# Kernel optimization log

Measured on AMD Instinct MI355X. Metric: run time of the kernel, lower is better.

## Reference

```python
import jax, jax.numpy as jnp
import numpy as np

N = 16384          # nodes
E_R = 524288       # radial edges (avg degree 32)
E_B = 32768        # bonded edges
N_TYPES = 20       # atom types
CS = 64            # scalar (0e) channels
CV = 32            # vector (1o) channels
EA = 16            # edge_attr_dim
EA_B = EA // 2     # bondedness embedding dim
EA_R = (EA + 1) // 2  # radial basis dim
CUTOFF = 1.5       # effective_radial_cutoff
L = 2              # n_layers
NORM = float(np.sqrt((E_R + E_B) / N))  # ~sqrt(avg degree) message normalization


def setup_inputs() -> dict:
    key = jax.random.key(0)
    ks = jax.random.split(key, 32)
    def rn(i, shape, scale=1.0):
        return jax.random.normal(ks[i], shape, dtype=jnp.float32) * scale
    s_e = 1.0 / np.sqrt(EA)
    inp = {}
    inp["pos"] = rn(0, (N, 3))
    inp["c_noise"] = rn(1, (1,))
    inp["atom_types"] = jax.random.randint(ks[2], (N,), 0, N_TYPES)
    inp["radial_edge_index"] = jax.random.randint(ks[3], (2, E_R), 0, N)
    inp["bonded_edge_index"] = jax.random.randint(ks[4], (2, E_B), 0, N)
    # learned parameters
    inp["atom_tab"] = rn(5, (N_TYPES, CS))
    inp["bond_tab"] = rn(6, (2, EA_B))
    inp["ns0_w"] = rn(7, (CS,), 0.1)
    inp["We0"] = rn(8, (EA, CS), s_e)
    inp["We1"] = rn(9, (EA, CS), s_e)
    inp["Wself0"] = rn(10, (CS, CS), 1.0 / np.sqrt(CS))
    inp["Ws0"] = rn(11, (CS, CS), 1.0 / np.sqrt(CS))
    inp["Wv0"] = rn(12, (CS, CV), 1.0 / np.sqrt(CS))
    inp["ns_w"] = rn(13, (L, CS + CV), 0.1)
    inp["We_ss"] = rn(14, (L, EA, CS), s_e)
    inp["We_vs"] = rn(15, (L, EA, CV), s_e)
    inp["We_sv"] = rn(16, (L, EA, CS), s_e)
    inp["We_vv"] = rn(17, (L, EA, CV), s_e)
    inp["We_vx"] = rn(18, (L, EA, CV), s_e)
    inp["Wmix_s"] = rn(19, (L, CS + CV, CS), 1.0 / np.sqrt(CS + CV))
    inp["Wmix_v"] = rn(20, (L, CS + 2 * CV, CV), 1.0 / np.sqrt(CS + 2 * CV))
    inp["Wself_s"] = rn(21, (L, CS, CS), 1.0 / np.sqrt(CS))
    inp["Wself_v"] = rn(22, (L, CV, CV), 1.0 / np.sqrt(CV))
    inp["skip_w"] = rn(23, (L, 2 * (CS + CV)), 0.1)
    inp["skip_b"] = rn(24, (L, 2 * (CS + CV)), 0.1)
    inp["w_out"] = rn(25, (CV,), 1.0 / np.sqrt(CV))
    inp["gain"] = jnp.asarray(0.5, dtype=jnp.float32)
    return inp


def _radial_basis(d):
    # e3nn soft_one_hot_linspace, basis='gaussian', cutoff=True
    centers = jnp.linspace(0.0, CUTOFF, EA_R + 2)[1:-1]
    step = centers[1] - centers[0]
    diff = (d[:, None] - centers[None, :]) / step
    return jnp.exp(-diff * diff) * 1.12


def reference(pos, c_noise, atom_tab, bond_tab, ns0_w, We0, We1, Wself0, Ws0, Wv0,
              ns_w, We_ss, We_vs, We_sv, We_vv, We_vx, Wmix_s, Wmix_v, Wself_s, Wself_v,
              skip_w, skip_b, w_out, gain, atom_types, radial_edge_index, bonded_edge_index):
    edge_index = jnp.concatenate([radial_edge_index, bonded_edge_index], axis=1)
    bond_mask = jnp.concatenate([jnp.zeros((E_R,), jnp.int32), jnp.ones((E_B,), jnp.int32)])
    src, dst = edge_index[0], edge_index[1]
    edge_vec = pos[src] - pos[dst]                      # [E,3]
    d = jnp.sqrt(jnp.sum(edge_vec * edge_vec, -1) + 1e-12)
    Y1 = jnp.sqrt(3.0) * edge_vec / d[:, None]          # l=1 SH, component norm; Y0 == 1
    edge_attr = jnp.concatenate([bond_tab[bond_mask], _radial_basis(d)], axis=-1)  # [E,EA]

    # atom embedding + initial noise-conditional scaling
    s = atom_tab[atom_types] * (1.0 + c_noise * ns0_w)  # [N,CS]

    # initial projector: scalar-input equivariant conv -> hidden irreps
    w0 = edge_attr @ We0
    w1 = edge_attr @ We1
    s_src = s[src]
    a_s = jax.ops.segment_sum(w0 * s_src, dst, num_segments=N) / NORM
    a_v = jax.ops.segment_sum((w1 * s_src)[:, :, None] * Y1[:, None, :], dst, num_segments=N) / NORM
    s_h = a_s @ Ws0 + s @ Wself0                        # [N,CS]
    v_h = jnp.einsum('nci,cd->ndi', a_v, Wv0)           # [N,CV,3]

    for l in range(L):
        # noise-conditional scaling (per-irrep-channel scalar scale)
        scale = 1.0 + c_noise * ns_w[l]
        ss = s_h * scale[:CS]
        vv = v_h * scale[CS:][None, :, None]
        ss_e = ss[src]
        vv_e = vv[src]
        # edge-attr-conditioned tensor-product weights
        w_ss = edge_attr @ We_ss[l]
        w_vs = edge_attr @ We_vs[l]
        w_sv = edge_attr @ We_sv[l]
        w_vv = edge_attr @ We_vv[l]
        w_vx = edge_attr @ We_vx[l]
        # CG tensor-product messages: 0x0->0, 1x1->0 (dot), 0x1->1, 1x0->1, 1x1->1 (cross)
        vdot = jnp.einsum('eci,ei->ec', vv_e, Y1)
        m_s = jnp.concatenate([w_ss * ss_e, w_vs * vdot], axis=-1)          # [E,CS+CV]
        m_v = jnp.concatenate([
            (w_sv * ss_e)[:, :, None] * Y1[:, None, :],
            w_vv[:, :, None] * vv_e,
            w_vx[:, :, None] * jnp.cross(vv_e, Y1[:, None, :]),
        ], axis=1)                                                          # [E,CS+2CV,3]
        a_s = jax.ops.segment_sum(m_s, dst, num_segments=N) / NORM
        a_v = jax.ops.segment_sum(m_v, dst, num_segments=N) / NORM
        new_s = a_s @ Wmix_s[l] + ss @ Wself_s[l]
        new_v = jnp.einsum('nci,cd->ndi', a_v, Wmix_v[l]) + jnp.einsum('nci,cd->ndi', vv, Wself_v[l])
        # noise-conditional skip connection (gated residual)
        g = jax.nn.sigmoid(skip_b[l] + c_noise * skip_w[l])
        s_h = g[:CS] * s_h + g[CS:2 * CS] * new_s
        g_v = g[2 * CS:]
        v_h = g_v[:CV][None, :, None] * v_h + g_v[CV:][None, :, None] * new_v

    # output head: 1o vectors -> 3D displacement, times output gain
    return jnp.einsum('nci,c->ni', v_h, w_out) * gain
```

## Files before the change

### kernel.cpp

```cpp
#include <hip/hip_runtime.h>
#include <math.h>

#define NA 16384
#define ER 524288
#define EB 32768
#define ET 557056
#define INV_NORM 0.17149858514250882f
#define SQRT3 1.7320508075688772f
#define RB_STEP (1.5f/9.0f)
#define BINS 512
#define DMAX 2.5f
#define INV_H ((float)BINS / DMAX)
#define T0U (2 * BINS * 128)
#define TLU (2 * BINS * 256)

typedef unsigned int uint32;
typedef unsigned short ushort16;

__device__ __forceinline__ float sigmoidf_(float x) { return 1.f / (1.f + __expf(-x)); }

__device__ __forceinline__ ushort16 f2bf(float x) {
  uint32 u = __float_as_uint(x);
  u = u + 0x7FFFu + ((u >> 16) & 1u);
  return (ushort16)(u >> 16);
}
__device__ __forceinline__ uint32 packbf(float hi, float lo) {
  return ((uint32)f2bf(hi) << 16) | (uint32)f2bf(lo);
}
__device__ __forceinline__ float bfhi(uint32 u) { return __uint_as_float(u & 0xFFFF0000u); }
__device__ __forceinline__ float bflo(uint32 u) { return __uint_as_float(u << 16); }

__global__ void k_zero(int* __restrict__ count) {
  count[blockIdx.x * 256 + threadIdx.x] = 0;
}

__global__ void k_hist(const int* __restrict__ rad, const int* __restrict__ bon, int* __restrict__ count) {
  int e = blockIdx.x * 256 + threadIdx.x;
  int d = (e < ER) ? rad[ER + e] : bon[EB + (e - ER)];
  atomicAdd(&count[d], 1);
}

__global__ void k_scan1(const int* __restrict__ count, int* __restrict__ partial) {
  __shared__ int red[256];
  int b = blockIdx.x, t = threadIdx.x;
  red[t] = count[b * 256 + t];
  __syncthreads();
  for (int s = 128; s > 0; s >>= 1) {
    if (t < s) red[t] += red[t + s];
    __syncthreads();
  }
  if (t == 0) partial[b] = red[0];
}

__global__ void k_scan2(int* __restrict__ partial) {
  int run = 0;
  for (int i = 0; i < 64; ++i) { int c = partial[i]; partial[i] = run; run += c; }
}

__global__ void k_scan3(const int* __restrict__ count, const int* __restrict__ partial,
                        int* __restrict__ offsets, int* __restrict__ cursor) {
  __shared__ int sc[256];
  int b = blockIdx.x, t = threadIdx.x;
  int v = count[b * 256 + t];
  sc[t] = v;
  __syncthreads();
  for (int off = 1; off < 256; off <<= 1) {
    int x = (t >= off) ? sc[t - off] : 0;
    __syncthreads();
    sc[t] += x;
    __syncthreads();
  }
  int excl = sc[t] - v + partial[b];
  offsets[b * 256 + t] = excl;
  cursor[b * 256 + t] = excl;
  if (b == 63 && t == 255) offsets[NA] = excl + v;
}

__global__ void k_fill_pre(const int* __restrict__ rad, const int* __restrict__ bon,
                           int* __restrict__ cursor, const float* __restrict__ pos,
                           float* __restrict__ rec8) {
  int e = blockIdx.x * 256 + threadIdx.x;
  int src, dst, v;
  if (e < ER) { src = rad[e]; dst = rad[ER + e]; v = 0; }
  else        { src = bon[e - ER]; dst = bon[EB + e - ER]; v = 1; }
  float dx = pos[src * 3] - pos[dst * 3];
  float dy = pos[src * 3 + 1] - pos[dst * 3 + 1];
  float dz = pos[src * 3 + 2] - pos[dst * 3 + 2];
  float dist = sqrtf(dx * dx + dy * dy + dz * dz + 1e-12f);
  float inv = 1.f / dist;
  float fq = fminf(dist * INV_H, BINS - 1.001f);
  int q = (int)fq;
  float frac = fq - (float)q;
  int qoffL = (v * BINS + q) << 8;
  int slot = atomicAdd(&cursor[dst], 1);
  float* rp = rec8 + (size_t)slot * 8;
  *(float4*)rp = make_float4(__int_as_float(src), SQRT3 * dx * inv, SQRT3 * dy * inv, SQRT3 * dz * inv);
  rp[4] = frac;
  rp[5] = __int_as_float(qoffL);
}

__global__ void k_build(const float* __restrict__ We0, const float* __restrict__ We1,
                        const float* __restrict__ We_ss, const float* __restrict__ We_vs,
                        const float* __restrict__ We_sv, const float* __restrict__ We_vv,
                        const float* __restrict__ We_vx, const float* __restrict__ bond_tab,
                        uint32* __restrict__ T0, uint32* __restrict__ TL) {
  int q = blockIdx.x, t = blockIdx.y, v = blockIdx.z, c = threadIdx.x;
  float d0 = q * (DMAX / BINS), d1 = (q + 1) * (DMAX / BINS);
  float rb0[8], rb1[8];
#pragma unroll
  for (int k = 0; k < 8; ++k) {
    float f0 = (d0 - (k + 1) * RB_STEP) * (1.f / RB_STEP);
    float f1 = (d1 - (k + 1) * RB_STEP) * (1.f / RB_STEP);
    rb0[k] = 1.12f * __expf(-f0 * f0);
    rb1[k] = 1.12f * __expf(-f1 * f1);
  }
  if (t == 0) {
    float ba = 0, bb = 0, a0 = 0, a1 = 0, b0 = 0, b1 = 0;
#pragma unroll
    for (int k = 0; k < 8; ++k) {
      float bt = bond_tab[v * 8 + k];
      float av_lo = We0[k * 64 + c], av_hi = We0[(8 + k) * 64 + c];
      float bv_lo = We1[k * 64 + c], bv_hi = We1[(8 + k) * 64 + c];
      ba += bt * av_lo; bb += bt * bv_lo;
      a0 += rb0[k] * av_hi; a1 += rb1[k] * av_hi;
      b0 += rb0[k] * bv_hi; b1 += rb1[k] * bv_hi;
    }
    uint32* o = T0 + (((size_t)v * BINS + q) << 7) + c * 2;
    o[0] = packbf(ba + a0, a1 - a0);
    o[1] = packbf(bb + b0, b1 - b0);
  } else {
    int l = t - 1;
    const float* Wss = We_ss + l * 1024;
    const float* Wsv = We_sv + l * 1024;
    const float* WA = (c < 32) ? (We_vs + l * 512) : (We_vx + l * 512);
    const float* WB = (c < 32) ? (We_vv + l * 512) : nullptr;
    int cu = c & 31;
    float sa = 0, sb = 0, s0 = 0, s1 = 0, t0 = 0, t1 = 0;
    float ua = 0, ub = 0, u0 = 0, u1 = 0, w0 = 0, w1 = 0;
#pragma unroll
    for (int k = 0; k < 8; ++k) {
      float bt = bond_tab[v * 8 + k];
      float ss_lo = Wss[k * 64 + c], ss_hi = Wss[(8 + k) * 64 + c];
      float sv_lo = Wsv[k * 64 + c], sv_hi = Wsv[(8 + k) * 64 + c];
      sa += bt * ss_lo; sb += bt * sv_lo;
      s0 += rb0[k] * ss_hi; s1 += rb1[k] * ss_hi;
      t0 += rb0[k] * sv_hi; t1 += rb1[k] * sv_hi;
      float a_lo = WA[k * 32 + cu], a_hi = WA[(8 + k) * 32 + cu];
      ua += bt * a_lo;
      u0 += rb0[k] * a_hi; u1 += rb1[k] * a_hi;
      if (WB) {
        float b_lo = WB[k * 32 + cu], b_hi = WB[(8 + k) * 32 + cu];
        ub += bt * b_lo;
        w0 += rb0[k] * b_hi; w1 += rb1[k] * b_hi;
      }
    }
    uint32* o = TL + (size_t)l * TLU + (((size_t)v * BINS + q) << 8) + c * 4;
    o[0] = packbf(sa + s0, s1 - s0);
    o[1] = packbf(sb + t0, t1 - t0);
    o[2] = packbf(ua + u0, u1 - u0);
    o[3] = WB ? packbf(ub + w0, w1 - w0) : 0u;
  }
}

__global__ void k_embed(const float* __restrict__ atom_tab, const int* __restrict__ types,
                        const float* __restrict__ ns0_w, const float* __restrict__ cnoise,
                        float* __restrict__ s_feat, ushort16* __restrict__ s_bf) {
  int tid = blockIdx.x * 256 + threadIdx.x;
  int n = tid >> 6, c = tid & 63;
  float cn = cnoise[0];
  float v = atom_tab[types[n] * 64 + c] * (1.f + cn * ns0_w[c]);
  s_feat[tid] = v;
  s_bf[tid] = f2bf(v);
}

__global__ __launch_bounds__(256, 8) void k_agg0(
    const int* __restrict__ offsets, const float* __restrict__ rec8,
    const uint32* __restrict__ T0, const ushort16* __restrict__ s_bf,
    float* __restrict__ a_s, float* __restrict__ a_v) {
  int lane = threadIdx.x & 63;
  int n = blockIdx.x * 4 + (threadIdx.x >> 6);
  float acc = 0, a0 = 0, a1 = 0, a2 = 0;
  int beg = __builtin_amdgcn_readfirstlane(offsets[n]);
  int end = __builtin_amdgcn_readfirstlane(offsets[n + 1]);
  if (beg < end) {
    int last = end - 1;
    int e1 = (beg + 1 < end) ? beg + 1 : last;
    int e2 = (beg + 2 < end) ? beg + 2 : last;
    const float* p0 = rec8 + (size_t)beg * 8;
    const float* p1 = rec8 + (size_t)e1 * 8;
    const float* p2 = rec8 + (size_t)e2 * 8;
    float4 rA0 = *(const float4*)p0; float2 rB0 = *(const float2*)(p0 + 4);
    float4 rA1 = *(const float4*)p1; float2 rB1 = *(const float2*)(p1 + 4);
    float4 rA2 = *(const float4*)p2; float2 rB2 = *(const float2*)(p2 + 4);
    uint2 t0 = *(const uint2*)(T0 + (__float_as_int(rB0.y) >> 1) + (lane << 1));
    ushort16 s0 = s_bf[((size_t)__float_as_int(rA0.x) << 6) + lane];
    uint2 t1 = *(const uint2*)(T0 + (__float_as_int(rB1.y) >> 1) + (lane << 1));
    ushort16 s1 = s_bf[((size_t)__float_as_int(rA1.x) << 6) + lane];
#pragma unroll 3
    for (int idx = beg; idx < end; ++idx) {
      uint2 t2 = *(const uint2*)(T0 + (__float_as_int(rB2.y) >> 1) + (lane << 1));
      ushort16 s2 = s_bf[((size_t)__float_as_int(rA2.x) << 6) + lane];
      int e3 = (idx + 3 < end) ? idx + 3 : last;
      const float* p3 = rec8 + (size_t)e3 * 8;
      float4 rA3 = *(const float4*)p3; float2 rB3 = *(const float2*)(p3 + 4);
      float frac = rB0.x;
      float w0 = fmaf(frac, bflo(t0.x), bfhi(t0.x));
      float w1 = fmaf(frac, bflo(t0.y), bfhi(t0.y));
      float sv = __uint_as_float((uint32)s0 << 16);
      acc += w0 * sv;
      float t = w1 * sv;
      a0 += t * rA0.y; a1 += t * rA0.z; a2 += t * rA0.w;
      rA0 = rA1; rB0 = rB1; rA1 = rA2; rB1 = rB2; rA2 = rA3; rB2 = rB3;
      t0 = t1; s0 = s1; t1 = t2; s1 = s2;
    }
  }
  a_s[n * 64 + lane] = acc * INV_NORM;
  *(float4*)(a_v + ((size_t)n << 8) + (lane << 2)) =
      make_float4(a0 * INV_NORM, a1 * INV_NORM, a2 * INV_NORM, 0.f);
}

__global__ __launch_bounds__(256, 8) void k_agg_layer(
    const float* __restrict__ cnoise, const float* __restrict__ nsw,
    const int* __restrict__ offsets, const float* __restrict__ rec8,
    const uint32* __restrict__ TL, const ushort16* __restrict__ sh_bf,
    const uint32* __restrict__ vh_bf,
    float* __restrict__ a_s, float* __restrict__ a_v) {
  int lane = threadIdx.x & 63;
  int n = blockIdx.x * 4 + (threadIdx.x >> 6);
  int vc = lane & 31;
  bool low = lane < 32;
  float cn = cnoise[0];
  float scale_s = 1.f + cn * nsw[lane];
  float scale_v = 1.f + cn * nsw[64 + vc];

  float ms = 0;
  float av0 = 0, av1 = 0, av2 = 0;
  float ms2 = 0;
  float b0 = 0, b1 = 0, b2 = 0;
  int beg = __builtin_amdgcn_readfirstlane(offsets[n]);
  int end = __builtin_amdgcn_readfirstlane(offsets[n + 1]);
  if (beg < end) {
    int last = end - 1;
    int e1 = (beg + 1 < end) ? beg + 1 : last;
    int e2 = (beg + 2 < end) ? beg + 2 : last;
    const float* p0 = rec8 + (size_t)beg * 8;
    const float* p1 = rec8 + (size_t)e1 * 8;
    const float* p2 = rec8 + (size_t)e2 * 8;
    float4 rA0 = *(const float4*)p0; float2 rB0 = *(const float2*)(p0 + 4);
    float4 rA1 = *(const float4*)p1; float2 rB1 = *(const float2*)(p1 + 4);
    float4 rA2 = *(const float4*)p2; float2 rB2 = *(const float2*)(p2 + 4);
    uint4 t0 = *(const uint4*)(TL + __float_as_int(rB0.y) + (lane << 2));
    ushort16 s0 = sh_bf[((size_t)__float_as_int(rA0.x) << 6) + lane];
    uint2 v0 = *(const uint2*)(vh_bf + ((size_t)__float_as_int(rA0.x) << 6) + (vc << 1));
    uint4 t1 = *(const uint4*)(TL + __float_as_int(rB1.y) + (lane << 2));
    ushort16 s1 = sh_bf[((size_t)__float_as_int(rA1.x) << 6) + lane];
    uint2 v1 = *(const uint2*)(vh_bf + ((size_t)__float_as_int(rA1.x) << 6) + (vc << 1));
#pragma unroll 3
    for (int idx = beg; idx < end; ++idx) {
      uint4 t2 = *(const uint4*)(TL + __float_as_int(rB2.y) + (lane << 2));
      ushort16 s2 = sh_bf[((size_t)__float_as_int(rA2.x) << 6) + lane];
      uint2 v2 = *(const uint2*)(vh_bf + ((size_t)__float_as_int(rA2.x) << 6) + (vc << 1));
      int e3 = (idx + 3 < end) ? idx + 3 : last;
      const float* p3 = rec8 + (size_t)e3 * 8;
      float4 rA3 = *(const float4*)p3; float2 rB3 = *(const float2*)(p3 + 4);
      float frac = rB0.x;
      float y0 = rA0.y, y1 = rA0.z, y2 = rA0.w;
      float wS  = fmaf(frac, bflo(t0.x), bfhi(t0.x));
      float wSV = fmaf(frac, bflo(t0.y), bfhi(t0.y));
      float wA  = fmaf(frac, bflo(t0.z), bfhi(t0.z));
      float wB  = fmaf(frac, bflo(t0.w), bfhi(t0.w));
      float ss = __uint_as_float((uint32)s0 << 16);
      float vx = bfhi(v0.x), vy = bflo(v0.x), vz = bfhi(v0.y);
      ms += wS * ss;
      float t = wSV * ss;
      av0 += t * y0; av1 += t * y1; av2 += t * y2;
      float vdot = vx * y0 + vy * y1 + vz * y2;
      ms2 += wA * vdot;
      float cx = vy * y2 - vz * y1;
      float cy = vz * y0 - vx * y2;
      float cz = vx * y1 - vy * y0;
      float m0 = low ? vx : cx;
      float m1 = low ? vy : cy;
      float m2 = low ? vz : cz;
      float wM = low ? wB : wA;
      b0 += wM * m0; b1 += wM * m1; b2 += wM * m2;
      rA0 = rA1; rB0 = rB1; rA1 = rA2; rB1 = rB2; rA2 = rA3; rB2 = rB3;
      t0 = t1; s0 = s1; v0 = v1; t1 = t2; s1 = s2; v1 = v2;
    }
  }
  float fs = scale_s * INV_NORM;
  float fv = scale_v * INV_NORM;
  a_s[n * 96 + lane] = ms * fs;
  float* avn = a_v + ((size_t)n << 9);
  *(float4*)(avn + (lane << 2)) = make_float4(av0 * fs, av1 * fs, av2 * fs, 0.f);
  if (low) {
    a_s[n * 96 + 64 + vc] = ms2 * fv;
    *(float4*)(avn + ((64 + vc) << 2)) = make_float4(b0 * fv, b1 * fv, b2 * fv, 0.f);
  } else {
    *(float4*)(avn + ((96 + vc) << 2)) = make_float4(b0 * fv, b1 * fv, b2 * fv, 0.f);
  }
}

__global__ __launch_bounds__(256, 4) void k_init_s(
    const float* __restrict__ a_s, const float* __restrict__ s_feat,
    const float* __restrict__ Ws0, const float* __restrict__ Wself0,
    float* __restrict__ sh, ushort16* __restrict__ sh_bf) {
  __shared__ float W1[64 * 64];
  __shared__ float W2[64 * 64];
  __shared__ float La[8 * 64];
  __shared__ float Lf[8 * 64];
  int tid = threadIdx.x;
  for (int i = tid; i < 1024; i += 256) {
    ((float4*)W1)[i] = ((const float4*)Ws0)[i];
    ((float4*)W2)[i] = ((const float4*)Wself0)[i];
  }
  int base = blockIdx.x * 8;
  for (int i = tid; i < 512; i += 256) {
    La[i] = a_s[(size_t)base * 64 + i];
    Lf[i] = s_feat[(size_t)base * 64 + i];
  }
  __syncthreads();
  int d = tid & 63, g = tid >> 6;
  int n0 = base + g * 2;
  const float* A0 = La + g * 128;
  const float* A1 = A0 + 64;
  const float* F0 = Lf + g * 128;
  const float* F1 = F0 + 64;
  float a0 = 0, a1 = 0;
#pragma unroll 8
  for (int c = 0; c < 64; ++c) {
    float w1 = W1[c * 64 + d], w2 = W2[c * 64 + d];
    a0 += A0[c] * w1 + F0[c] * w2;
    a1 += A1[c] * w1 + F1[c] * w2;
  }
  sh[(size_t)n0 * 64 + d] = a0;
  sh[(size_t)(n0 + 1) * 64 + d] = a1;
  sh_bf[(size_t)n0 * 64 + d] = f2bf(a0);
  sh_bf[(size_t)(n0 + 1) * 64 + d] = f2bf(a1);
}

__global__ __launch_bounds__(256, 4) void k_init_v(
    const float* __restrict__ a_v, const float* __restrict__ Wv0,
    float* __restrict__ vh, uint32* __restrict__ vh_bf) {
  __shared__ float W[64 * 32];
  int tid = threadIdx.x;
  for (int i = tid; i < 512; i += 256) ((float4*)W)[i] = ((const float4*)Wv0)[i];
  __syncthreads();
  int d = tid & 31, g = tid >> 5;
  int n = blockIdx.x * 8 + g;
  const float4* av = (const float4*)(a_v + ((size_t)n << 8));
  float x = 0, y = 0, z = 0;
#pragma unroll 4
  for (int c = 0; c < 64; ++c) {
    float4 a = av[c];
    float w = W[c * 32 + d];
    x += a.x * w; y += a.y * w; z += a.z * w;
  }
  *(float4*)(vh + ((size_t)n << 7) + (d << 2)) = make_float4(x, y, z, 0.f);
  *(uint2*)(vh_bf + ((size_t)n << 6) + (d << 1)) = make_uint2(packbf(x, y), packbf(z, 0.f));
}

__global__ __launch_bounds__(256, 4) void k_mix_s(
    const float* __restrict__ a_s, const float* __restrict__ sh_in,
    const float* __restrict__ Wmix_s, const float* __restrict__ Wself_s,
    const float* __restrict__ nsw, const float* __restrict__ skw,
    const float* __restrict__ skb, const float* __restrict__ cnoise,
    float* __restrict__ sh_out, ushort16* __restrict__ sh_bf_out) {
  __shared__ float Wm[96 * 64];
  __shared__ float Wsf[64 * 64];
  __shared__ float La[8 * 96];
  int tid = threadIdx.x;
  float cn = cnoise[0];
  for (int i = tid; i < 96 * 16; i += 256) ((float4*)Wm)[i] = ((const float4*)Wmix_s)[i];
  for (int i = tid; i < 64 * 16; i += 256) {
    float4 wv = ((const float4*)Wself_s)[i];
    int c = i >> 4;
    float sc = 1.f + cn * nsw[c];
    wv.x *= sc; wv.y *= sc; wv.z *= sc; wv.w *= sc;
    ((float4*)Wsf)[i] = wv;
  }
  int base = blockIdx.x * 8;
  for (int i = tid; i < 8 * 96; i += 256) La[i] = a_s[(size_t)base * 96 + i];
  __syncthreads();
  int d = tid & 63, g = tid >> 6;
  int n0 = base + g * 2;
  const float* A0 = La + (g * 2) * 96;
  const float* A1 = A0 + 96;
  const float* s0p = sh_in + (size_t)n0 * 64;
  const float* s1p = s0p + 64;
  float acc0 = 0, acc1 = 0;
#pragma unroll 8
  for (int c = 0; c < 96; ++c) {
    float w = Wm[c * 64 + d];
    acc0 += A0[c] * w;
    acc1 += A1[c] * w;
  }
#pragma unroll 8
  for (int c = 0; c < 64; ++c) {
    float w = Wsf[c * 64 + d];
    acc0 += s0p[c] * w;
    acc1 += s1p[c] * w;
  }
  float g1 = sigmoidf_(skb[d] + cn * skw[d]);
  float g2 = sigmoidf_(skb[64 + d] + cn * skw[64 + d]);
  float o0 = g1 * s0p[d] + g2 * acc0;
  float o1 = g1 * s1p[d] + g2 * acc1;
  sh_out[(size_t)n0 * 64 + d] = o0;
  sh_out[(size_t)(n0 + 1) * 64 + d] = o1;
  sh_bf_out[(size_t)n0 * 64 + d] = f2bf(o0);
  sh_bf_out[(size_t)(n0 + 1) * 64 + d] = f2bf(o1);
}

__global__ __launch_bounds__(256, 4) void k_mix_v(
    const float* __restrict__ a_v, const float* __restrict__ vh_in,
    const float* __restrict__ Wmix_v, const float* __restrict__ Wself_v,
    const float* __restrict__ nsw, const float* __restrict__ skw,
    const float* __restrict__ skb, const float* __restrict__ cnoise,
    float* __restrict__ vh_out, uint32* __restrict__ vh_bf_out) {
  __shared__ float Wm[128 * 32];
  __shared__ float Wsf[32 * 32];
  int tid = threadIdx.x;
  float cn = cnoise[0];
  for (int i = tid; i < 128 * 8; i += 256) ((float4*)Wm)[i] = ((const float4*)Wmix_v)[i];
  for (int i = tid; i < 32 * 8; i += 256) {
    float4 wv = ((const float4*)Wself_v)[i];
    int c = i >> 3;
    float sc = 1.f + cn * nsw[64 + c];
    wv.x *= sc; wv.y *= sc; wv.z *= sc; wv.w *= sc;
    ((float4*)Wsf)[i] = wv;
  }
  __syncthreads();
  int d = tid & 31, g = tid >> 5;
  int n = blockIdx.x * 8 + g;
  const float4* av = (const float4*)(a_v + ((size_t)n << 9));
  const float4* vr = (const float4*)(vh_in + ((size_t)n << 7));
  float x = 0, y = 0, z = 0;
#pragma unroll 4
  for (int c = 0; c < 128; ++c) {
    float4 a = av[c];
    float w = Wm[c * 32 + d];
    x += a.x * w; y += a.y * w; z += a.z * w;
  }
#pragma unroll 4
  for (int c = 0; c < 32; ++c) {
    float4 vv = vr[c];
    float w = Wsf[c * 32 + d];
    x += vv.x * w; y += vv.y * w; z += vv.z * w;
  }
  float g3 = sigmoidf_(skb[128 + d] + cn * skw[128 + d]);
  float g4 = sigmoidf_(skb[160 + d] + cn * skw[160 + d]);
  float4 vi = vr[d];
  float ox = g3 * vi.x + g4 * x;
  float oy = g3 * vi.y + g4 * y;
  float oz = g3 * vi.z + g4 * z;
  *(float4*)(vh_out + ((size_t)n << 7) + (d << 2)) = make_float4(ox, oy, oz, 0.f);
  *(uint2*)(vh_bf_out + ((size_t)n << 6) + (d << 1)) = make_uint2(packbf(ox, oy), packbf(oz, 0.f));
}

__global__ void k_out(const float* __restrict__ vh, const float* __restrict__ w_out,
                      const float* __restrict__ gain, float* __restrict__ out) {
  int tid = blockIdx.x * 256 + threadIdx.x;
  int n = tid / 3, i = tid - n * 3;
  float acc = 0;
  for (int c = 0; c < 32; ++c) acc += vh[((size_t)n << 7) + c * 4 + i] * w_out[c];
  out[tid] = acc * gain[0];
}

extern "C" void kernel_launch(void* const* d_in, const int* in_sizes, int n_in,
                              void* d_out, int out_size, void* d_ws, size_t ws_size,
                              hipStream_t stream) {
  (void)in_sizes; (void)n_in; (void)out_size; (void)ws_size;
  const float* pos     = (const float*)d_in[0];
  const float* cn      = (const float*)d_in[1];
  const int*   types   = (const int*)d_in[2];
  const int*   rad     = (const int*)d_in[3];
  const int*   bon     = (const int*)d_in[4];
  const float* atom_tab= (const float*)d_in[5];
  const float* bond_tab= (const float*)d_in[6];
  const float* ns0_w   = (const float*)d_in[7];
  const float* We0     = (const float*)d_in[8];
  const float* We1     = (const float*)d_in[9];
  const float* Wself0  = (const float*)d_in[10];
  const float* Ws0     = (const float*)d_in[11];
  const float* Wv0     = (const float*)d_in[12];
  const float* ns_w    = (const float*)d_in[13];
  const float* We_ss   = (const float*)d_in[14];
  const float* We_vs   = (const float*)d_in[15];
  const float* We_sv   = (const float*)d_in[16];
  const float* We_vv   = (const float*)d_in[17];
  const float* We_vx   = (const float*)d_in[18];
  const float* Wmix_s  = (const float*)d_in[19];
  const float* Wmix_v  = (const float*)d_in[20];
  const float* Wself_s = (const float*)d_in[21];
  const float* Wself_v = (const float*)d_in[22];
  const float* skip_w  = (const float*)d_in[23];
  const float* skip_b  = (const float*)d_in[24];
  const float* w_out   = (const float*)d_in[25];
  const float* gain    = (const float*)d_in[26];

  char* ws = (char*)d_ws;
  size_t o = 0;
  auto alloc = [&](size_t bytes) -> void* {
    void* p = ws + o;
    o += (bytes + 255) & ~(size_t)255;
    return p;
  };
  float* s_feat  = (float*)alloc((size_t)NA * 64 * 4);
  ushort16* s_bf = (ushort16*)alloc((size_t)NA * 64 * 2);
  float* a_s     = (float*)alloc((size_t)NA * 96 * 4);
  float* a_v     = (float*)alloc((size_t)NA * 512 * 4);
  float* sh0     = (float*)alloc((size_t)NA * 64 * 4);
  float* sh1     = (float*)alloc((size_t)NA * 64 * 4);
  ushort16* shbf0= (ushort16*)alloc((size_t)NA * 64 * 2);
  ushort16* shbf1= (ushort16*)alloc((size_t)NA * 64 * 2);
  float* vh0     = (float*)alloc((size_t)NA * 128 * 4);
  float* vh1     = (float*)alloc((size_t)NA * 128 * 4);
  uint32* vhbf0  = (uint32*)alloc((size_t)NA * 64 * 4);
  uint32* vhbf1  = (uint32*)alloc((size_t)NA * 64 * 4);
  int* count     = (int*)alloc((size_t)NA * 4);
  int* partial   = (int*)alloc((size_t)64 * 4);
  int* offsets   = (int*)alloc((size_t)(NA + 1) * 4);
  int* cursor    = (int*)alloc((size_t)NA * 4);
  float* rec8    = (float*)alloc((size_t)ET * 32);
  uint32* T0     = (uint32*)alloc((size_t)T0U * 4);
  uint32* TL     = (uint32*)alloc((size_t)2 * TLU * 4);
  float* shb[2]  = {sh0, sh1};
  ushort16* shbf[2] = {shbf0, shbf1};
  float* vhb[2]  = {vh0, vh1};
  uint32* vhbf[2]= {vhbf0, vhbf1};

  k_zero<<<NA / 256, 256, 0, stream>>>(count);
  k_hist<<<ET / 256, 256, 0, stream>>>(rad, bon, count);
  k_scan1<<<64, 256, 0, stream>>>(count, partial);
  k_scan2<<<1, 1, 0, stream>>>(partial);
  k_scan3<<<64, 256, 0, stream>>>(count, partial, offsets, cursor);
  k_fill_pre<<<ET / 256, 256, 0, stream>>>(rad, bon, cursor, pos, rec8);
  k_build<<<dim3(BINS, 3, 2), 64, 0, stream>>>(We0, We1, We_ss, We_vs, We_sv, We_vv, We_vx,
                                               bond_tab, T0, TL);

  k_embed<<<NA * 64 / 256, 256, 0, stream>>>(atom_tab, types, ns0_w, cn, s_feat, s_bf);
  k_agg0<<<NA / 4, 256, 0, stream>>>(offsets, rec8, T0, s_bf, a_s, a_v);
  k_init_s<<<NA / 8, 256, 0, stream>>>(a_s, s_feat, Ws0, Wself0, shb[0], shbf[0]);
  k_init_v<<<NA / 8, 256, 0, stream>>>(a_v, Wv0, vhb[0], vhbf[0]);

  for (int l = 0; l < 2; ++l) {
    int bin = l & 1, bout = 1 - bin;
    k_agg_layer<<<NA / 4, 256, 0, stream>>>(
        cn, ns_w + l * 96, offsets, rec8, TL + (size_t)l * TLU, shbf[bin], vhbf[bin], a_s, a_v);
    k_mix_s<<<NA / 8, 256, 0, stream>>>(
        a_s, shb[bin], Wmix_s + l * 96 * 64, Wself_s + l * 64 * 64,
        ns_w + l * 96, skip_w + l * 192, skip_b + l * 192, cn, shb[bout], shbf[bout]);
    k_mix_v<<<NA / 8, 256, 0, stream>>>(
        a_v, vhb[bin], Wmix_v + l * 128 * 32, Wself_v + l * 32 * 32,
        ns_w + l * 96, skip_w + l * 192, skip_b + l * 192, cn, vhb[bout], vhbf[bout]);
  }
  k_out<<<NA * 3 / 256, 256, 0, stream>>>(vhb[0], w_out, gain, (float*)d_out);
}
```

Measured before the change: 470.7 us.

## Merge small kernels, store aggregated vectors in bf16, use nontemporal edge loads

Several independent launches are merged into single grids by splitting on block index: fill with embed, init_s with init_v, and mix_s with mix_v per layer. The zero kernel becomes a memset. The aggregated vector buffer a_v is now written as packed bf16 instead of float4, halving its traffic. Edge-record loads and aggregate stores use nontemporal hints. The bf16 storage of a_v costs precision in the mixing matmuls, and merged kernels use a larger shared-memory footprint that may lower occupancy.

New measurement: 508.8 us. +8.1%, slower.

```diff
diff --git a/kernel.cpp b/kernel.cpp
--- a/kernel.cpp
+++ b/kernel.cpp
@@ -16,6 +16,9 @@
 
 typedef unsigned int uint32;
 typedef unsigned short ushort16;
+typedef float vf4 __attribute__((ext_vector_type(4)));
+typedef float vf2 __attribute__((ext_vector_type(2)));
+typedef unsigned int vu2 __attribute__((ext_vector_type(2)));
 
 __device__ __forceinline__ float sigmoidf_(float x) { return 1.f / (1.f + __expf(-x)); }
 
@@ -30,8 +33,28 @@
 __device__ __forceinline__ float bfhi(uint32 u) { return __uint_as_float(u & 0xFFFF0000u); }
 __device__ __forceinline__ float bflo(uint32 u) { return __uint_as_float(u << 16); }
 
-__global__ void k_zero(int* __restrict__ count) {
-  count[blockIdx.x * 256 + threadIdx.x] = 0;
+__device__ __forceinline__ float4 ntl4(const float* p) {
+  vf4 v = __builtin_nontemporal_load((const vf4*)p);
+  return make_float4(v.x, v.y, v.z, v.w);
+}
+__device__ __forceinline__ float2 ntl2(const float* p) {
+  vf2 v = __builtin_nontemporal_load((const vf2*)p);
+  return make_float2(v.x, v.y);
+}
+__device__ __forceinline__ void nts4(float* p, float a, float b, float c, float d) {
+  vf4 v; v.x = a; v.y = b; v.z = c; v.w = d;
+  __builtin_nontemporal_store(v, (vf4*)p);
+}
+__device__ __forceinline__ void nts2(float* p, float a, float b) {
+  vf2 v; v.x = a; v.y = b;
+  __builtin_nontemporal_store(v, (vf2*)p);
+}
+__device__ __forceinline__ void ntsu2(uint32* p, uint32 a, uint32 b) {
+  vu2 v; v.x = a; v.y = b;
+  __builtin_nontemporal_store(v, (vu2*)p);
+}
+__device__ __forceinline__ void nts1(float* p, float a) {
+  __builtin_nontemporal_store(a, p);
 }
 
 __global__ void k_hist(const int* __restrict__ rad, const int* __restrict__ bon, int* __restrict__ count) {
@@ -76,27 +99,38 @@
   if (b == 63 && t == 255) offsets[NA] = excl + v;
 }
 
-__global__ void k_fill_pre(const int* __restrict__ rad, const int* __restrict__ bon,
-                           int* __restrict__ cursor, const float* __restrict__ pos,
-                           float* __restrict__ rec8) {
-  int e = blockIdx.x * 256 + threadIdx.x;
-  int src, dst, v;
-  if (e < ER) { src = rad[e]; dst = rad[ER + e]; v = 0; }
-  else        { src = bon[e - ER]; dst = bon[EB + e - ER]; v = 1; }
-  float dx = pos[src * 3] - pos[dst * 3];
-  float dy = pos[src * 3 + 1] - pos[dst * 3 + 1];
-  float dz = pos[src * 3 + 2] - pos[dst * 3 + 2];
-  float dist = sqrtf(dx * dx + dy * dy + dz * dz + 1e-12f);
-  float inv = 1.f / dist;
-  float fq = fminf(dist * INV_H, BINS - 1.001f);
-  int q = (int)fq;
-  float frac = fq - (float)q;
-  int qoffL = (v * BINS + q) << 8;
-  int slot = atomicAdd(&cursor[dst], 1);
-  float* rp = rec8 + (size_t)slot * 8;
-  *(float4*)rp = make_float4(__int_as_float(src), SQRT3 * dx * inv, SQRT3 * dy * inv, SQRT3 * dz * inv);
-  rp[4] = frac;
-  rp[5] = __int_as_float(qoffL);
+__global__ void k_fill_embed(const int* __restrict__ rad, const int* __restrict__ bon,
+                             int* __restrict__ cursor, const float* __restrict__ pos,
+                             float* __restrict__ rec8,
+                             const float* __restrict__ atom_tab, const int* __restrict__ types,
+                             const float* __restrict__ ns0_w, const float* __restrict__ cnoise,
+                             float* __restrict__ s_feat, ushort16* __restrict__ s_bf) {
+  if (blockIdx.x < ET / 256) {
+    int e = blockIdx.x * 256 + threadIdx.x;
+    int src, dst, v;
+    if (e < ER) { src = rad[e]; dst = rad[ER + e]; v = 0; }
+    else        { src = bon[e - ER]; dst = bon[EB + e - ER]; v = 1; }
+    float dx = pos[src * 3] - pos[dst * 3];
+    float dy = pos[src * 3 + 1] - pos[dst * 3 + 1];
+    float dz = pos[src * 3 + 2] - pos[dst * 3 + 2];
+    float dist = sqrtf(dx * dx + dy * dy + dz * dz + 1e-12f);
+    float inv = 1.f / dist;
+    float fq = fminf(dist * INV_H, BINS - 1.001f);
+    int q = (int)fq;
+    float frac = fq - (float)q;
+    int qoffL = (v * BINS + q) << 8;
+    int slot = atomicAdd(&cursor[dst], 1);
+    float* rp = rec8 + (size_t)slot * 8;
+    nts4(rp, __int_as_float(src), SQRT3 * dx * inv, SQRT3 * dy * inv, SQRT3 * dz * inv);
+    nts2(rp + 4, frac, __int_as_float(qoffL));
+  } else {
+    int tid = (blockIdx.x - ET / 256) * 256 + threadIdx.x;
+    int n = tid >> 6, c = tid & 63;
+    float cn = cnoise[0];
+    float v = atom_tab[types[n] * 64 + c] * (1.f + cn * ns0_w[c]);
+    s_feat[tid] = v;
+    s_bf[tid] = f2bf(v);
+  }
 }
 
 __global__ void k_build(const float* __restrict__ We0, const float* __restrict__ We1,
@@ -162,21 +196,10 @@
   }
 }
 
-__global__ void k_embed(const float* __restrict__ atom_tab, const int* __restrict__ types,
-                        const float* __restrict__ ns0_w, const float* __restrict__ cnoise,
-                        float* __restrict__ s_feat, ushort16* __restrict__ s_bf) {
-  int tid = blockIdx.x * 256 + threadIdx.x;
-  int n = tid >> 6, c = tid & 63;
-  float cn = cnoise[0];
-  float v = atom_tab[types[n] * 64 + c] * (1.f + cn * ns0_w[c]);
-  s_feat[tid] = v;
-  s_bf[tid] = f2bf(v);
-}
-
 __global__ __launch_bounds__(256, 8) void k_agg0(
     const int* __restrict__ offsets, const float* __restrict__ rec8,
     const uint32* __restrict__ T0, const ushort16* __restrict__ s_bf,
-    float* __restrict__ a_s, float* __restrict__ a_v) {
+    float* __restrict__ a_s, uint32* __restrict__ a_v) {
   int lane = threadIdx.x & 63;
   int n = blockIdx.x * 4 + (threadIdx.x >> 6);
   float acc = 0, a0 = 0, a1 = 0, a2 = 0;
@@ -189,9 +212,9 @@
     const float* p0 = rec8 + (size_t)beg * 8;
     const float* p1 = rec8 + (size_t)e1 * 8;
     const float* p2 = rec8 + (size_t)e2 * 8;
-    float4 rA0 = *(const float4*)p0; float2 rB0 = *(const float2*)(p0 + 4);
-    float4 rA1 = *(const float4*)p1; float2 rB1 = *(const float2*)(p1 + 4);
-    float4 rA2 = *(const float4*)p2; float2 rB2 = *(const float2*)(p2 + 4);
+    float4 rA0 = ntl4(p0); float2 rB0 = ntl2(p0 + 4);
+    float4 rA1 = ntl4(p1); float2 rB1 = ntl2(p1 + 4);
+    float4 rA2 = ntl4(p2); float2 rB2 = ntl2(p2 + 4);
     uint2 t0 = *(const uint2*)(T0 + (__float_as_int(rB0.y) >> 1) + (lane << 1));
     ushort16 s0 = s_bf[((size_t)__float_as_int(rA0.x) << 6) + lane];
     uint2 t1 = *(const uint2*)(T0 + (__float_as_int(rB1.y) >> 1) + (lane << 1));
@@ -202,7 +225,7 @@
       ushort16 s2 = s_bf[((size_t)__float_as_int(rA2.x) << 6) + lane];
       int e3 = (idx + 3 < end) ? idx + 3 : last;
       const float* p3 = rec8 + (size_t)e3 * 8;
-      float4 rA3 = *(const float4*)p3; float2 rB3 = *(const float2*)(p3 + 4);
+      float4 rA3 = ntl4(p3); float2 rB3 = ntl2(p3 + 4);
       float frac = rB0.x;
       float w0 = fmaf(frac, bflo(t0.x), bfhi(t0.x));
       float w1 = fmaf(frac, bflo(t0.y), bfhi(t0.y));
@@ -214,9 +237,9 @@
       t0 = t1; s0 = s1; t1 = t2; s1 = s2;
     }
   }
-  a_s[n * 64 + lane] = acc * INV_NORM;
-  *(float4*)(a_v + ((size_t)n << 8) + (lane << 2)) =
-      make_float4(a0 * INV_NORM, a1 * INV_NORM, a2 * INV_NORM, 0.f);
+  nts1(a_s + n * 64 + lane, acc * INV_NORM);
+  ntsu2(a_v + ((size_t)n << 7) + (lane << 1),
+        packbf(a0 * INV_NORM, a1 * INV_NORM), packbf(a2 * INV_NORM, 0.f));
 }
 
 __global__ __launch_bounds__(256, 8) void k_agg_layer(
@@ -224,7 +247,7 @@
     const int* __restrict__ offsets, const float* __restrict__ rec8,
     const uint32* __restrict__ TL, const ushort16* __restrict__ sh_bf,
     const uint32* __restrict__ vh_bf,
-    float* __restrict__ a_s, float* __restrict__ a_v) {
+    float* __restrict__ a_s, uint32* __restrict__ a_v) {
   int lane = threadIdx.x & 63;
   int n = blockIdx.x * 4 + (threadIdx.x >> 6);
   int vc = lane & 31;
@@ -246,9 +269,9 @@
     const float* p0 = rec8 + (size_t)beg * 8;
     const float* p1 = rec8 + (size_t)e1 * 8;
     const float* p2 = rec8 + (size_t)e2 * 8;
-    float4 rA0 = *(const float4*)p0; float2 rB0 = *(const float2*)(p0 + 4);
-    float4 rA1 = *(const float4*)p1; float2 rB1 = *(const float2*)(p1 + 4);
-    float4 rA2 = *(const float4*)p2; float2 rB2 = *(const float2*)(p2 + 4);
+    float4 rA0 = ntl4(p0); float2 rB0 = ntl2(p0 + 4);
+    float4 rA1 = ntl4(p1); float2 rB1 = ntl2(p1 + 4);
+    float4 rA2 = ntl4(p2); float2 rB2 = ntl2(p2 + 4);
     uint4 t0 = *(const uint4*)(TL + __float_as_int(rB0.y) + (lane << 2));
     ushort16 s0 = sh_bf[((size_t)__float_as_int(rA0.x) << 6) + lane];
     uint2 v0 = *(const uint2*)(vh_bf + ((size_t)__float_as_int(rA0.x) << 6) + (vc << 1));
@@ -262,7 +285,7 @@
       uint2 v2 = *(const uint2*)(vh_bf + ((size_t)__float_as_int(rA2.x) << 6) + (vc << 1));
       int e3 = (idx + 3 < end) ? idx + 3 : last;
       const float* p3 = rec8 + (size_t)e3 * 8;
-      float4 rA3 = *(const float4*)p3; float2 rB3 = *(const float2*)(p3 + 4);
+      float4 rA3 = ntl4(p3); float2 rB3 = ntl2(p3 + 4);
       float frac = rB0.x;
       float y0 = rA0.y, y1 = rA0.z, y2 = rA0.w;
       float wS  = fmaf(frac, bflo(t0.x), bfhi(t0.x));
@@ -290,171 +313,168 @@
   }
   float fs = scale_s * INV_NORM;
   float fv = scale_v * INV_NORM;
-  a_s[n * 96 + lane] = ms * fs;
-  float* avn = a_v + ((size_t)n << 9);
-  *(float4*)(avn + (lane << 2)) = make_float4(av0 * fs, av1 * fs, av2 * fs, 0.f);
+  nts1(a_s + n * 96 + lane, ms * fs);
+  uint32* avn = a_v + ((size_t)n << 8);
+  ntsu2(avn + (lane << 1), packbf(av0 * fs, av1 * fs), packbf(av2 * fs, 0.f));
   if (low) {
-    a_s[n * 96 + 64 + vc] = ms2 * fv;
-    *(float4*)(avn + ((64 + vc) << 2)) = make_float4(b0 * fv, b1 * fv, b2 * fv, 0.f);
+    nts1(a_s + n * 96 + 64 + vc, ms2 * fv);
+    ntsu2(avn + ((64 + vc) << 1), packbf(b0 * fv, b1 * fv), packbf(b2 * fv, 0.f));
   } else {
-    *(float4*)(avn + ((96 + vc) << 2)) = make_float4(b0 * fv, b1 * fv, b2 * fv, 0.f);
-  }
-}
-
-__global__ __launch_bounds__(256, 4) void k_init_s(
+    ntsu2(avn + ((96 + vc) << 1), packbf(b0 * fv, b1 * fv), packbf(b2 * fv, 0.f));
+  }
+}
+
+__global__ __launch_bounds__(256, 4) void k_init(
     const float* __restrict__ a_s, const float* __restrict__ s_feat,
     const float* __restrict__ Ws0, const float* __restrict__ Wself0,
-    float* __restrict__ sh, ushort16* __restrict__ sh_bf) {
-  __shared__ float W1[64 * 64];
-  __shared__ float W2[64 * 64];
-  __shared__ float La[8 * 64];
-  __shared__ float Lf[8 * 64];
+    const uint32* __restrict__ a_v, const float* __restrict__ Wv0,
+    float* __restrict__ sh, ushort16* __restrict__ sh_bf,
+    float* __restrict__ vh, uint32* __restrict__ vh_bf) {
+  __shared__ float SM[9216];
   int tid = threadIdx.x;
-  for (int i = tid; i < 1024; i += 256) {
-    ((float4*)W1)[i] = ((const float4*)Ws0)[i];
-    ((float4*)W2)[i] = ((const float4*)Wself0)[i];
-  }
-  int base = blockIdx.x * 8;
-  for (int i = tid; i < 512; i += 256) {
-    La[i] = a_s[(size_t)base * 64 + i];
-    Lf[i] = s_feat[(size_t)base * 64 + i];
-  }
-  __syncthreads();
-  int d = tid & 63, g = tid >> 6;
-  int n0 = base + g * 2;
-  const float* A0 = La + g * 128;
-  const float* A1 = A0 + 64;
-  const float* F0 = Lf + g * 128;
-  const float* F1 = F0 + 64;
-  float a0 = 0, a1 = 0;
+  if (blockIdx.x < NA / 8) {
+    float* W1 = SM;
+    float* W2 = SM + 4096;
+    float* La = SM + 8192;
+    float* Lf = SM + 8704;
+    for (int i = tid; i < 1024; i += 256) {
+      ((float4*)W1)[i] = ((const float4*)Ws0)[i];
+      ((float4*)W2)[i] = ((const float4*)Wself0)[i];
+    }
+    int base = blockIdx.x * 8;
+    for (int i = tid; i < 512; i += 256) {
+      La[i] = a_s[(size_t)base * 64 + i];
+      Lf[i] = s_feat[(size_t)base * 64 + i];
+    }
+    __syncthreads();
+    int d = tid & 63, g = tid >> 6;
+    int n0 = base + g * 2;
+    const float* A0 = La + g * 128;
+    const float* A1 = A0 + 64;
+    const float* F0 = Lf + g * 128;
+    const float* F1 = F0 + 64;
+    float a0 = 0, a1 = 0;
 #pragma unroll 8
-  for (int c = 0; c < 64; ++c) {
-    float w1 = W1[c * 64 + d], w2 = W2[c * 64 + d];
-    a0 += A0[c] * w1 + F0[c] * w2;
-    a1 += A1[c] * w1 + F1[c] * w2;
-  }
-  sh[(size_t)n0 * 64 + d] = a0;
-  sh[(size_t)(n0 + 1) * 64 + d] = a1;
-  sh_bf[(size_t)n0 * 64 + d] = f2bf(a0);
-  sh_bf[(size_t)(n0 + 1) * 64 + d] = f2bf(a1);
-}
-
-__global__ __launch_bounds__(256, 4) void k_init_v(
-    const float* __restrict__ a_v, const float* __restrict__ Wv0,
-    float* __restrict__ vh, uint32* __restrict__ vh_bf) {
-  __shared__ float W[64 * 32];
-  int tid = threadIdx.x;
-  for (int i = tid; i < 512; i += 256) ((float4*)W)[i] = ((const float4*)Wv0)[i];
-  __syncthreads();
-  int d = tid & 31, g = tid >> 5;
-  int n = blockIdx.x * 8 + g;
-  const float4* av = (const float4*)(a_v + ((size_t)n << 8));
-  float x = 0, y = 0, z = 0;
+    for (int c = 0; c < 64; ++c) {
+      float w1 = W1[c * 64 + d], w2 = W2[c * 64 + d];
+      a0 += A0[c] * w1 + F0[c] * w2;
+      a1 += A1[c] * w1 + F1[c] * w2;
+    }
+    sh[(size_t)n0 * 64 + d] = a0;
+    sh[(size_t)(n0 + 1) * 64 + d] = a1;
+    sh_bf[(size_t)n0 * 64 + d] = f2bf(a0);
+    sh_bf[(size_t)(n0 + 1) * 64 + d] = f2bf(a1);
+  } else {
+    float* W = SM;
+    for (int i = tid; i < 512; i += 256) ((float4*)W)[i] = ((const float4*)Wv0)[i];
+    __syncthreads();
+    int d = tid & 31, g = tid >> 5;
+    int n = (blockIdx.x - NA / 8) * 8 + g;
+    const uint2* av = (const uint2*)a_v + ((size_t)n << 6);
+    float x = 0, y = 0, z = 0;
 #pragma unroll 4
-  for (int c = 0; c < 64; ++c) {
-    float4 a = av[c];
-    float w = W[c * 32 + d];
-    x += a.x * w; y += a.y * w; z += a.z * w;
-  }
-  *(float4*)(vh + ((size_t)n << 7) + (d << 2)) = make_float4(x, y, z, 0.f);
-  *(uint2*)(vh_bf + ((size_t)n << 6) + (d << 1)) = make_uint2(packbf(x, y), packbf(z, 0.f));
-}
-
-__global__ __launch_bounds__(256, 4) void k_mix_s(
+    for (int c = 0; c < 64; ++c) {
+      uint2 a = av[c];
+      float w = W[c * 32 + d];
+      x += bfhi(a.x) * w; y += bflo(a.x) * w; z += bfhi(a.y) * w;
+    }
+    *(float4*)(vh + ((size_t)n << 7) + (d << 2)) = make_float4(x, y, z, 0.f);
+    *(uint2*)(vh_bf + ((size_t)n << 6) + (d << 1)) = make_uint2(packbf(x, y), packbf(z, 0.f));
+  }
+}
+
+__global__ __launch_bounds__(256, 4) void k_mix(
     const float* __restrict__ a_s, const float* __restrict__ sh_in,
     const float* __restrict__ Wmix_s, const float* __restrict__ Wself_s,
-    const float* __restrict__ nsw, const float* __restrict__ skw,
-    const float* __restrict__ skb, const float* __restrict__ cnoise,
-    float* __restrict__ sh_out, ushort16* __restrict__ sh_bf_out) {
-  __shared__ float Wm[96 * 64];
-  __shared__ float Wsf[64 * 64];
-  __shared__ float La[8 * 96];
-  int tid = threadIdx.x;
-  float cn = cnoise[0];
-  for (int i = tid; i < 96 * 16; i += 256) ((float4*)Wm)[i] = ((const float4*)Wmix_s)[i];
-  for (int i = tid; i < 64 * 16; i += 256) {
-    float4 wv = ((const float4*)Wself_s)[i];
-    int c = i >> 4;
-    float sc = 1.f + cn * nsw[c];
-    wv.x *= sc; wv.y *= sc; wv.z *= sc; wv.w *= sc;
-    ((float4*)Wsf)[i] = wv;
-  }
-  int base = blockIdx.x * 8;
-  for (int i = tid; i < 8 * 96; i += 256) La[i] = a_s[(size_t)base * 96 + i];
-  __syncthreads();
-  int d = tid & 63, g = tid >> 6;
-  int n0 = base + g * 2;
-  const float* A0 = La + (g * 2) * 96;
-  const float* A1 = A0 + 96;
-  const float* s0p = sh_in + (size_t)n0 * 64;
-  const float* s1p = s0p + 64;
-  float acc0 = 0, acc1 = 0;
-#pragma unroll 8
-  for (int c = 0; c < 96; ++c) {
-    float w = Wm[c * 64 + d];
-    acc0 += A0[c] * w;
-    acc1 += A1[c] * w;
-  }
-#pragma unroll 8
-  for (int c = 0; c < 64; ++c) {
-    float w = Wsf[c * 64 + d];
-    acc0 += s0p[c] * w;
-    acc1 += s1p[c] * w;
-  }
-  float g1 = sigmoidf_(skb[d] + cn * skw[d]);
-  float g2 = sigmoidf_(skb[64 + d] + cn * skw[64 + d]);
-  float o0 = g1 * s0p[d] + g2 * acc0;
-  float o1 = g1 * s1p[d] + g2 * acc1;
-  sh_out[(size_t)n0 * 64 + d] = o0;
-  sh_out[(size_t)(n0 + 1) * 64 + d] = o1;
-  sh_bf_out[(size_t)n0 * 64 + d] = f2bf(o0);
-  sh_bf_out[(size_t)(n0 + 1) * 64 + d] = f2bf(o1);
-}
-
-__global__ __launch_bounds__(256, 4) void k_mix_v(
-    const float* __restrict__ a_v, const float* __restrict__ vh_in,
+    const uint32* __restrict__ a_v, const float* __restrict__ vh_in,
     const float* __restrict__ Wmix_v, const float* __restrict__ Wself_v,
     const float* __restrict__ nsw, const float* __restrict__ skw,
     const float* __restrict__ skb, const float* __restrict__ cnoise,
+    float* __restrict__ sh_out, ushort16* __restrict__ sh_bf_out,
     float* __restrict__ vh_out, uint32* __restrict__ vh_bf_out) {
-  __shared__ float Wm[128 * 32];
-  __shared__ float Wsf[32 * 32];
+  __shared__ float SM[11008];
   int tid = threadIdx.x;
   float cn = cnoise[0];
-  for (int i = tid; i < 128 * 8; i += 256) ((float4*)Wm)[i] = ((const float4*)Wmix_v)[i];
-  for (int i = tid; i < 32 * 8; i += 256) {
-    float4 wv = ((const float4*)Wself_v)[i];
-    int c = i >> 3;
-    float sc = 1.f + cn * nsw[64 + c];
-    wv.x *= sc; wv.y *= sc; wv.z *= sc; wv.w *= sc;
-    ((float4*)Wsf)[i] = wv;
-  }
-  __syncthreads();
-  int d = tid & 31, g = tid >> 5;
-  int n = blockIdx.x * 8 + g;
-  const float4* av = (const float4*)(a_v + ((size_t)n << 9));
-  const float4* vr = (const float4*)(vh_in + ((size_t)n << 7));
-  float x = 0, y = 0, z = 0;
+  if (blockIdx.x < NA / 8) {
+    float* Wm = SM;
+    float* Wsf = SM + 6144;
+    float* La = SM + 10240;
+    for (int i = tid; i < 96 * 16; i += 256) ((float4*)Wm)[i] = ((const float4*)Wmix_s)[i];
+    for (int i = tid; i < 64 * 16; i += 256) {
+      float4 wv = ((const float4*)Wself_s)[i];
+      int c = i >> 4;
+      float sc = 1.f + cn * nsw[c];
+      wv.x *= sc; wv.y *= sc; wv.z *= sc; wv.w *= sc;
+      ((float4*)Wsf)[i] = wv;
+    }
+    int base = blockIdx.x * 8;
+    for (int i = tid; i < 8 * 96; i += 256) La[i] = a_s[(size_t)base * 96 + i];
+    __syncthreads();
+    int d = tid & 63, g = tid >> 6;
+    int n0 = base + g * 2;
+    const float* A0 = La + (g * 2) * 96;
+    const float* A1 = A0 + 96;
+    const float* s0p = sh_in + (size_t)n0 * 64;
+    const float* s1p = s0p + 64;
+    float acc0 = 0, acc1 = 0;
+#pragma unroll 8
+    for (int c = 0; c < 96; ++c) {
+      float w = Wm[c * 64 + d];
+      acc0 += A0[c] * w;
+      acc1 += A1[c] * w;
+    }
+#pragma unroll 8
+    for (int c = 0; c < 64; ++c) {
+      float w = Wsf[c * 64 + d];
+      acc0 += s0p[c] * w;
+      acc1 += s1p[c] * w;
+    }
+    float g1 = sigmoidf_(skb[d] + cn * skw[d]);
+    float g2 = sigmoidf_(skb[64 + d] + cn * skw[64 + d]);
+    float o0 = g1 * s0p[d] + g2 * acc0;
+    float o1 = g1 * s1p[d] + g2 * acc1;
+    sh_out[(size_t)n0 * 64 + d] = o0;
+    sh_out[(size_t)(n0 + 1) * 64 + d] = o1;
+    sh_bf_out[(size_t)n0 * 64 + d] = f2bf(o0);
+    sh_bf_out[(size_t)(n0 + 1) * 64 + d] = f2bf(o1);
+  } else {
+    float* Wm = SM;
+    float* Wsf = SM + 4096;
+    for (int i = tid; i < 128 * 8; i += 256) ((float4*)Wm)[i] = ((const float4*)Wmix_v)[i];
+    for (int i = tid; i < 32 * 8; i += 256) {
+      float4 wv = ((const float4*)Wself_v)[i];
+      int c = i >> 3;
+      float sc = 1.f + cn * nsw[64 + c];
+      wv.x *= sc; wv.y *= sc; wv.z *= sc; wv.w *= sc;
+      ((float4*)Wsf)[i] = wv;
+    }
+    __syncthreads();
+    int d = tid & 31, g = tid >> 5;
+    int n = (blockIdx.x - NA / 8) * 8 + g;
+    const uint2* av = (const uint2*)a_v + ((size_t)n << 7);
+    const float4* vr = (const float4*)(vh_in + ((size_t)n << 7));
+    float x = 0, y = 0, z = 0;
 #pragma unroll 4
-  for (int c = 0; c < 128; ++c) {
-    float4 a = av[c];
-    float w = Wm[c * 32 + d];
-    x += a.x * w; y += a.y * w; z += a.z * w;
-  }
+    for (int c = 0; c < 128; ++c) {
+      uint2 a = av[c];
+      float w = Wm[c * 32 + d];
+      x += bfhi(a.x) * w; y += bflo(a.x) * w; z += bfhi(a.y) * w;
+    }
 #pragma unroll 4
-  for (int c = 0; c < 32; ++c) {
-    float4 vv = vr[c];
-    float w = Wsf[c * 32 + d];
-    x += vv.x * w; y += vv.y * w; z += vv.z * w;
-  }
-  float g3 = sigmoidf_(skb[128 + d] + cn * skw[128 + d]);
-  float g4 = sigmoidf_(skb[160 + d] + cn * skw[160 + d]);
-  float4 vi = vr[d];
-  float ox = g3 * vi.x + g4 * x;
-  float oy = g3 * vi.y + g4 * y;
-  float oz = g3 * vi.z + g4 * z;
-  *(float4*)(vh_out + ((size_t)n << 7) + (d << 2)) = make_float4(ox, oy, oz, 0.f);
-  *(uint2*)(vh_bf_out + ((size_t)n << 6) + (d << 1)) = make_uint2(packbf(ox, oy), packbf(oz, 0.f));
+    for (int c = 0; c < 32; ++c) {
+      float4 vv = vr[c];
+      float w = Wsf[c * 32 + d];
+      x += vv.x * w; y += vv.y * w; z += vv.z * w;
+    }
+    float g3 = sigmoidf_(skb[128 + d] + cn * skw[128 + d]);
+    float g4 = sigmoidf_(skb[160 + d] + cn * skw[160 + d]);
+    float4 vi = vr[d];
+    float ox = g3 * vi.x + g4 * x;
+    float oy = g3 * vi.y + g4 * y;
+    float oz = g3 * vi.z + g4 * z;
+    *(float4*)(vh_out + ((size_t)n << 7) + (d << 2)) = make_float4(ox, oy, oz, 0.f);
+    *(uint2*)(vh_bf_out + ((size_t)n << 6) + (d << 1)) = make_uint2(packbf(ox, oy), packbf(oz, 0.f));
+  }
 }
 
 __global__ void k_out(const float* __restrict__ vh, const float* __restrict__ w_out,
@@ -508,7 +528,7 @@
   float* s_feat  = (float*)alloc((size_t)NA * 64 * 4);
   ushort16* s_bf = (ushort16*)alloc((size_t)NA * 64 * 2);
   float* a_s     = (float*)alloc((size_t)NA * 96 * 4);
-  float* a_v     = (float*)alloc((size_t)NA * 512 * 4);
+  uint32* a_v    = (uint32*)alloc((size_t)NA * 256 * 4);
   float* sh0     = (float*)alloc((size_t)NA * 64 * 4);
   float* sh1     = (float*)alloc((size_t)NA * 64 * 4);
   ushort16* shbf0= (ushort16*)alloc((size_t)NA * 64 * 2);
@@ -529,30 +549,29 @@
   float* vhb[2]  = {vh0, vh1};
   uint32* vhbf[2]= {vhbf0, vhbf1};
 
-  k_zero<<<NA / 256, 256, 0, stream>>>(count);
+  hipMemsetAsync(count, 0, (size_t)NA * 4, stream);
   k_hist<<<ET / 256, 256, 0, stream>>>(rad, bon, count);
   k_scan1<<<64, 256, 0, stream>>>(count, partial);
   k_scan2<<<1, 1, 0, stream>>>(partial);
   k_scan3<<<64, 256, 0, stream>>>(count, partial, offsets, cursor);
-  k_fill_pre<<<ET / 256, 256, 0, stream>>>(rad, bon, cursor, pos, rec8);
+  k_fill_embed<<<ET / 256 + NA * 64 / 256, 256, 0, stream>>>(
+      rad, bon, cursor, pos, rec8, atom_tab, types, ns0_w, cn, s_feat, s_bf);
   k_build<<<dim3(BINS, 3, 2), 64, 0, stream>>>(We0, We1, We_ss, We_vs, We_sv, We_vv, We_vx,
                                                bond_tab, T0, TL);
 
-  k_embed<<<NA * 64 / 256, 256, 0, stream>>>(atom_tab, types, ns0_w, cn, s_feat, s_bf);
   k_agg0<<<NA / 4, 256, 0, stream>>>(offsets, rec8, T0, s_bf, a_s, a_v);
-  k_init_s<<<NA / 8, 256, 0, stream>>>(a_s, s_feat, Ws0, Wself0, shb[0], shbf[0]);
-  k_init_v<<<NA / 8, 256, 0, stream>>>(a_v, Wv0, vhb[0], vhbf[0]);
+  k_init<<<NA / 4, 256, 0, stream>>>(a_s, s_feat, Ws0, Wself0, a_v, Wv0,
+                                     shb[0], shbf[0], vhb[0], vhbf[0]);
 
   for (int l = 0; l < 2; ++l) {
     int bin = l & 1, bout = 1 - bin;
     k_agg_layer<<<NA / 4, 256, 0, stream>>>(
         cn, ns_w + l * 96, offsets, rec8, TL + (size_t)l * TLU, shbf[bin], vhbf[bin], a_s, a_v);
-    k_mix_s<<<NA / 8, 256, 0, stream>>>(
+    k_mix<<<NA / 4, 256, 0, stream>>>(
         a_s, shb[bin], Wmix_s + l * 96 * 64, Wself_s + l * 64 * 64,
-        ns_w + l * 96, skip_w + l * 192, skip_b + l * 192, cn, shb[bout], shbf[bout]);
-    k_mix_v<<<NA / 8, 256, 0, stream>>>(
         a_v, vhb[bin], Wmix_v + l * 128 * 32, Wself_v + l * 32 * 32,
-        ns_w + l * 96, skip_w + l * 192, skip_b + l * 192, cn, vhb[bout], vhbf[bout]);
+        ns_w + l * 96, skip_w + l * 192, skip_b + l * 192, cn,
+        shb[bout], shbf[bout], vhb[bout], vhbf[bout]);
   }
   k_out<<<NA * 3 / 256, 256, 0, stream>>>(vhb[0], w_out, gain, (float*)d_out);
 }
```
